# Kernel optimization log

Hardware: AMD Instinct MI355X
Metric: run time of the kernel (lower is better)

## Reference

```python
import jax, jax.numpy as jnp
import numpy as np

HID = 4
IN = 150
LAYERS = 4
OUT = 1
SEQ = 512
BATCH = 256


def setup_inputs() -> dict:
    key = jax.random.key(0)
    ks = jax.random.split(key, 12)
    s = 1.0 / np.sqrt(HID)  # PyTorch LSTM init scale
    inp = {
        "x": jax.random.normal(ks[0], (SEQ, BATCH, IN), dtype=jnp.float32),
        "w_ih0": jax.random.uniform(ks[1], (4 * HID, IN), minval=-s, maxval=s, dtype=jnp.float32),
        "w_hh0": jax.random.uniform(ks[2], (4 * HID, HID), minval=-s, maxval=s, dtype=jnp.float32),
        "b_ih0": jax.random.uniform(ks[3], (4 * HID,), minval=-s, maxval=s, dtype=jnp.float32),
        "b_hh0": jax.random.uniform(ks[4], (4 * HID,), minval=-s, maxval=s, dtype=jnp.float32),
        "w_ih_rest": jax.random.uniform(ks[5], (LAYERS - 1, 4 * HID, HID), minval=-s, maxval=s, dtype=jnp.float32),
        "w_hh_rest": jax.random.uniform(ks[6], (LAYERS - 1, 4 * HID, HID), minval=-s, maxval=s, dtype=jnp.float32),
        "b_ih_rest": jax.random.uniform(ks[7], (LAYERS - 1, 4 * HID), minval=-s, maxval=s, dtype=jnp.float32),
        "b_hh_rest": jax.random.uniform(ks[8], (LAYERS - 1, 4 * HID), minval=-s, maxval=s, dtype=jnp.float32),
        "fc_w": jax.random.uniform(ks[9], (OUT, HID), minval=-s, maxval=s, dtype=jnp.float32),
        "fc_b": jax.random.uniform(ks[10], (OUT,), minval=-s, maxval=s, dtype=jnp.float32),
    }
    return inp


def _lstm_layer(x, w_ih, w_hh, b_ih, b_hh):
    # x: (S, B, D_in). PyTorch gate order: i, f, g, o.
    B = x.shape[1]
    xp = jnp.einsum('sbd,gd->sbg', x, w_ih) + (b_ih + b_hh)  # (S, B, 4H)

    def step(carry, xt):
        h, c = carry
        gates = xt + h @ w_hh.T  # (B, 4H)
        i, f, g, o = jnp.split(gates, 4, axis=-1)
        i = jax.nn.sigmoid(i)
        f = jax.nn.sigmoid(f)
        g = jnp.tanh(g)
        o = jax.nn.sigmoid(o)
        c = f * c + i * g
        h = o * jnp.tanh(c)
        return (h, c), h

    h0 = jnp.zeros((B, HID), dtype=x.dtype)
    c0 = jnp.zeros((B, HID), dtype=x.dtype)
    _, hs = jax.lax.scan(step, (h0, c0), xp)
    return hs  # (S, B, H)


def reference(x, w_ih0, w_hh0, b_ih0, b_hh0, w_ih_rest, w_hh_rest, b_ih_rest, b_hh_rest, fc_w, fc_b):
    h = _lstm_layer(x, w_ih0, w_hh0, b_ih0, b_hh0)
    for l in range(LAYERS - 1):
        h = _lstm_layer(h, w_ih_rest[l], w_hh_rest[l], b_ih_rest[l], b_hh_rest[l])
    s, b, hd = h.shape
    out = h.reshape(s * b, hd) @ fc_w.T + fc_b  # (S*B, OUT)
    return out.reshape(s, b, -1)
```

## Files before the change

kernel.cpp:

```cpp
#include <hip/hip_runtime.h>
#include <hip/hip_bf16.h>

#define SEQ 512
#define BATCH 256
#define IN_DIM 150

#if __has_builtin(__builtin_amdgcn_exp2f)
__device__ __forceinline__ float fexp2(float x){ return __builtin_amdgcn_exp2f(x); }
#else
__device__ __forceinline__ float fexp2(float x){ return exp2f(x); }
#endif
#if __has_builtin(__builtin_amdgcn_rcpf)
__device__ __forceinline__ float frcp(float x){ return __builtin_amdgcn_rcpf(x); }
#else
__device__ __forceinline__ float frcp(float x){ return 1.0f/(x); }
#endif

__device__ __forceinline__ float sigm(float x){ return frcp(1.0f + fexp2(-1.44269504088896341f*x)); }
__device__ __forceinline__ float tanhx(float x){ return 1.0f - 2.0f*frcp(1.0f + fexp2(2.88539008177792681f*x)); }

template<int CTRL>
__device__ __forceinline__ float dppmov(float v){
    return __int_as_float(__builtin_amdgcn_mov_dpp(__float_as_int(v), CTRL, 0xF, 0xF, true));
}

__global__ __launch_bounds__(256) void xproj(const float* __restrict__ x,
                                             const float* __restrict__ w,
                                             const float* __restrict__ bih,
                                             const float* __restrict__ bhh,
                                             float* __restrict__ xp)
{
    __shared__ float wl[16*IN_DIM];
    __shared__ float bl[16];
    for (int i=threadIdx.x; i<16*IN_DIM; i+=256) wl[i] = w[i];
    if (threadIdx.x < 16) bl[threadIdx.x] = bih[threadIdx.x] + bhh[threadIdx.x];
    __syncthreads();

    const int r = blockIdx.x*256 + threadIdx.x;
    const float* xr = x + (size_t)r*IN_DIM;
    float acc[16];
#pragma unroll
    for (int g=0; g<16; ++g) acc[g] = bl[g];
#pragma unroll 5
    for (int dq=0; dq<IN_DIM/2; ++dq) {
        const float2 xv = *(const float2*)(xr + dq*2);
#pragma unroll
        for (int g=0; g<16; ++g) {
            const float2 wv = *(const float2*)(&wl[g*IN_DIM + dq*2]);
            acc[g] += xv.x*wv.x + xv.y*wv.y;
        }
    }
    float4* op = (float4*)(xp + (size_t)r*16);
#pragma unroll
    for (int kk=0; kk<4; ++kk)
        op[kk] = make_float4(acc[kk], acc[4+kk], acc[8+kk], acc[12+kk]);
}

__global__ __launch_bounds__(64) void lstm_pipe(
    const float* __restrict__ xp,
    const float* __restrict__ w_hh0,
    const float* __restrict__ w_ih_r,
    const float* __restrict__ w_hh_r,
    const float* __restrict__ b_ih_r,
    const float* __restrict__ b_hh_r,
    const float* __restrict__ fcw,
    const float* __restrict__ fcb,
    float* __restrict__ out)
{
    const int lane = threadIdx.x;
    const int k  = lane & 3;
    const int l  = (lane >> 2) & 3;
    const int bb = lane >> 4;
    const int b  = blockIdx.x*4 + bb;

    const float* whh = (l==0) ? w_hh0 : (w_hh_r + (size_t)(l-1)*64);
    float whp[4][4], wir[4][4], bias[4], fcp[4];
#pragma unroll
    for (int j=0;j<4;++j) {
        const int row = j*4+k;
#pragma unroll
        for (int m=0;m<4;++m) whp[j][m] = whh[row*4 + (k^m)];
        if (l==0) {
            bias[j] = 0.f;
#pragma unroll
            for (int m=0;m<4;++m) wir[j][m] = (m==j) ? 1.f : 0.f;
        } else {
            const float* wih = w_ih_r + (size_t)(l-1)*64;
            bias[j] = b_ih_r[(l-1)*16+row] + b_hh_r[(l-1)*16+row];
#pragma unroll
            for (int m=0;m<4;++m) wir[j][m] = wih[row*4 + (k^m)];
        }
    }
#pragma unroll
    for (int m=0;m<4;++m) fcp[m] = fcw[k^m];
    const float fcbv = fcb[0];

    const float* xbase = xp + (size_t)b*16 + k*4;

    float h=0.f, c=0.f;
    float a0=0.f,a1=0.f,a2=0.f,a3=0.f;
    float s0=0.f,s1=0.f,s2=0.f,s3=0.f;

    auto LDX = [&](int t)->float4 {
        const int tc = t < SEQ-1 ? t : SEQ-1;
        return *(const float4*)(xbase + (size_t)tc*(BATCH*16));
    };

    auto STEP = [&](float4 xv, int tau) {
        const float x0 = (l==0) ? xv.x : s0;
        const float x1 = (l==0) ? xv.y : s1;
        const float x2 = (l==0) ? xv.z : s2;
        const float x3 = (l==0) ? xv.w : s3;
        float g0 = (bias[0] + ((wir[0][0]*x0 + wir[0][1]*x1) + (wir[0][2]*x2 + wir[0][3]*x3)))
                 + ((whp[0][0]*a0 + whp[0][1]*a1) + (whp[0][2]*a2 + whp[0][3]*a3));
        float g1 = (bias[1] + ((wir[1][0]*x0 + wir[1][1]*x1) + (wir[1][2]*x2 + wir[1][3]*x3)))
                 + ((whp[1][0]*a0 + whp[1][1]*a1) + (whp[1][2]*a2 + whp[1][3]*a3));
        float g2 = (bias[2] + ((wir[2][0]*x0 + wir[2][1]*x1) + (wir[2][2]*x2 + wir[2][3]*x3)))
                 + ((whp[2][0]*a0 + whp[2][1]*a1) + (whp[2][2]*a2 + whp[2][3]*a3));
        float g3 = (bias[3] + ((wir[3][0]*x0 + wir[3][1]*x1) + (wir[3][2]*x2 + wir[3][3]*x3)))
                 + ((whp[3][0]*a0 + whp[3][1]*a1) + (whp[3][2]*a2 + whp[3][3]*a3));
        const float ig = sigm(g0);
        const float fg = sigm(g1);
        const float gg = tanhx(g2);
        const float og = sigm(g3);
        c = fg*c + ig*gg;
        h = og * tanhx(c);
        const int t = tau - l;
        if (t < 0) { h = 0.f; c = 0.f; }
        a0 = h;
        a1 = dppmov<0xB1>(h);
        a2 = dppmov<0x4E>(h);
        a3 = dppmov<0x1B>(h);
        s0 = dppmov<0x114>(a0);
        s1 = dppmov<0x114>(a1);
        s2 = dppmov<0x114>(a2);
        s3 = dppmov<0x114>(a3);
        if (l==3 && k==0 && t >= 0 && t < SEQ) {
            out[(size_t)t*BATCH + b] =
                fcbv + ((fcp[0]*a0 + fcp[1]*a1) + (fcp[2]*a2 + fcp[3]*a3));
        }
    };

    float4 A0=LDX(0), A1=LDX(1), A2=LDX(2), A3=LDX(3);
    for (int tau=0; tau<520; tau+=8) {
        float4 B0=LDX(tau+4), B1=LDX(tau+5), B2=LDX(tau+6), B3=LDX(tau+7);
        STEP(A0,tau);   STEP(A1,tau+1); STEP(A2,tau+2); STEP(A3,tau+3);
        A0=LDX(tau+8);  A1=LDX(tau+9);  A2=LDX(tau+10); A3=LDX(tau+11);
        STEP(B0,tau+4); STEP(B1,tau+5); STEP(B2,tau+6); STEP(B3,tau+7);
    }
}

extern "C" void kernel_launch(void* const* d_in, const int* in_sizes, int n_in,
                              void* d_out, int out_size, void* d_ws, size_t ws_size,
                              hipStream_t stream)
{
    const float* x      = (const float*)d_in[0];
    const float* w_ih0  = (const float*)d_in[1];
    const float* w_hh0  = (const float*)d_in[2];
    const float* b_ih0  = (const float*)d_in[3];
    const float* b_hh0  = (const float*)d_in[4];
    const float* w_ih_r = (const float*)d_in[5];
    const float* w_hh_r = (const float*)d_in[6];
    const float* b_ih_r = (const float*)d_in[7];
    const float* b_hh_r = (const float*)d_in[8];
    const float* fc_w   = (const float*)d_in[9];
    const float* fc_b   = (const float*)d_in[10];
    float* out = (float*)d_out;

    float* xp0 = (float*)d_ws;

    xproj<<<SEQ*BATCH/256, 256, 0, stream>>>(x, w_ih0, b_ih0, b_hh0, xp0);
    lstm_pipe<<<BATCH/4, 64, 0, stream>>>(xp0, w_hh0, w_ih_r, w_hh_r,
                                          b_ih_r, b_hh_r, fc_w, fc_b, out);
}
```

Measured before the change: 270.1 us.

## Interleave two batch groups per wave and prescale gate weights into exp2 domain

```diff
diff --git a/kernel.cpp b/kernel.cpp
--- a/kernel.cpp
+++ b/kernel.cpp
@@ -16,47 +16,106 @@
 __device__ __forceinline__ float frcp(float x){ return 1.0f/(x); }
 #endif
 
-__device__ __forceinline__ float sigm(float x){ return frcp(1.0f + fexp2(-1.44269504088896341f*x)); }
-__device__ __forceinline__ float tanhx(float x){ return 1.0f - 2.0f*frcp(1.0f + fexp2(2.88539008177792681f*x)); }
+#define NEG_LOG2E -1.44269504088896341f
+#define TWO_LOG2E  2.88539008177792681f
 
 template<int CTRL>
 __device__ __forceinline__ float dppmov(float v){
     return __int_as_float(__builtin_amdgcn_mov_dpp(__float_as_int(v), CTRL, 0xF, 0xF, true));
 }
 
-__global__ __launch_bounds__(256) void xproj(const float* __restrict__ x,
-                                             const float* __restrict__ w,
-                                             const float* __restrict__ bih,
-                                             const float* __restrict__ bhh,
-                                             float* __restrict__ xp)
-{
-    __shared__ float wl[16*IN_DIM];
-    __shared__ float bl[16];
-    for (int i=threadIdx.x; i<16*IN_DIM; i+=256) wl[i] = w[i];
-    if (threadIdx.x < 16) bl[threadIdx.x] = bih[threadIdx.x] + bhh[threadIdx.x];
+#define XROWS 64
+__global__ __launch_bounds__(256) void xproj2(const float* __restrict__ x,
+                                              const float* __restrict__ w,
+                                              const float* __restrict__ bih,
+                                              const float* __restrict__ bhh,
+                                              float* __restrict__ xp)
+{
+    __shared__ float xs[XROWS*IN_DIM];
+    __shared__ float ws[16*IN_DIM];
+    __shared__ float bs[16];
+
+    for (int i=threadIdx.x; i<16*IN_DIM; i+=256) ws[i] = w[i];
+    if (threadIdx.x < 16) bs[threadIdx.x] = bih[threadIdx.x] + bhh[threadIdx.x];
+
+    const size_t tilebase = (size_t)blockIdx.x * XROWS * IN_DIM;
+    const float2* xg  = (const float2*)(x + tilebase);
+    float2*       xs2 = (float2*)xs;
+    for (int i=threadIdx.x; i<XROWS*(IN_DIM/2); i+=256) xs2[i] = xg[i];
     __syncthreads();
 
-    const int r = blockIdx.x*256 + threadIdx.x;
-    const float* xr = x + (size_t)r*IN_DIM;
-    float acc[16];
-#pragma unroll
-    for (int g=0; g<16; ++g) acc[g] = bl[g];
+    const int q = threadIdx.x & 3;
+    const int r = threadIdx.x >> 2;
+    float acc0 = bs[q], acc1 = bs[4+q], acc2 = bs[8+q], acc3 = bs[12+q];
+    const float* xr = xs + r*IN_DIM;
+    const float* w0p = ws + (q    )*IN_DIM;
+    const float* w1p = ws + (q+ 4 )*IN_DIM;
+    const float* w2p = ws + (q+ 8 )*IN_DIM;
+    const float* w3p = ws + (q+12 )*IN_DIM;
 #pragma unroll 5
-    for (int dq=0; dq<IN_DIM/2; ++dq) {
-        const float2 xv = *(const float2*)(xr + dq*2);
-#pragma unroll
-        for (int g=0; g<16; ++g) {
-            const float2 wv = *(const float2*)(&wl[g*IN_DIM + dq*2]);
-            acc[g] += xv.x*wv.x + xv.y*wv.y;
-        }
-    }
-    float4* op = (float4*)(xp + (size_t)r*16);
-#pragma unroll
-    for (int kk=0; kk<4; ++kk)
-        op[kk] = make_float4(acc[kk], acc[4+kk], acc[8+kk], acc[12+kk]);
-}
-
-__global__ __launch_bounds__(64) void lstm_pipe(
+    for (int d=0; d<IN_DIM/2; ++d) {
+        const float2 xv = *(const float2*)(xr  + 2*d);
+        const float2 w0 = *(const float2*)(w0p + 2*d);
+        const float2 w1 = *(const float2*)(w1p + 2*d);
+        const float2 w2 = *(const float2*)(w2p + 2*d);
+        const float2 w3 = *(const float2*)(w3p + 2*d);
+        acc0 += xv.x*w0.x + xv.y*w0.y;
+        acc1 += xv.x*w1.x + xv.y*w1.y;
+        acc2 += xv.x*w2.x + xv.y*w2.y;
+        acc3 += xv.x*w3.x + xv.y*w3.y;
+    }
+    const float4 o = make_float4(acc0*NEG_LOG2E, acc1*NEG_LOG2E,
+                                 acc2*TWO_LOG2E, acc3*NEG_LOG2E);
+    *(float4*)(xp + ((size_t)(blockIdx.x*XROWS + r))*16 + q*4) = o;
+}
+
+template<int PHASE>
+__device__ __forceinline__ void lstm_step(
+    float& h, float& c,
+    float& a0, float& a1, float& a2, float& a3,
+    float& s0, float& s1, float& s2, float& s3,
+    const float4 xv, const int tau, const int l, const int k, const int b,
+    const float wir[4][4], const float whp[4][4], const float bias[4],
+    const float fcp[4], const float fcbv, float* __restrict__ out)
+{
+    const float x0 = (l==0) ? xv.x : s0;
+    const float x1 = (l==0) ? xv.y : s1;
+    const float x2 = (l==0) ? xv.z : s2;
+    const float x3 = (l==0) ? xv.w : s3;
+    float g0 = (bias[0] + ((wir[0][0]*x0 + wir[0][1]*x1) + (wir[0][2]*x2 + wir[0][3]*x3)))
+             + ((whp[0][0]*a0 + whp[0][1]*a1) + (whp[0][2]*a2 + whp[0][3]*a3));
+    float g1 = (bias[1] + ((wir[1][0]*x0 + wir[1][1]*x1) + (wir[1][2]*x2 + wir[1][3]*x3)))
+             + ((whp[1][0]*a0 + whp[1][1]*a1) + (whp[1][2]*a2 + whp[1][3]*a3));
+    float g2 = (bias[2] + ((wir[2][0]*x0 + wir[2][1]*x1) + (wir[2][2]*x2 + wir[2][3]*x3)))
+             + ((whp[2][0]*a0 + whp[2][1]*a1) + (whp[2][2]*a2 + whp[2][3]*a3));
+    float g3 = (bias[3] + ((wir[3][0]*x0 + wir[3][1]*x1) + (wir[3][2]*x2 + wir[3][3]*x3)))
+             + ((whp[3][0]*a0 + whp[3][1]*a1) + (whp[3][2]*a2 + whp[3][3]*a3));
+    const float ig = frcp(1.0f + fexp2(g0));
+    const float fg = frcp(1.0f + fexp2(g1));
+    const float rg = frcp(1.0f + fexp2(g2));
+    const float og = frcp(1.0f + fexp2(g3));
+    const float gg = __builtin_fmaf(-2.0f, rg, 1.0f);
+    c = __builtin_fmaf(fg, c, ig*gg);
+    const float rc = frcp(1.0f + fexp2(TWO_LOG2E*c));
+    h = og * __builtin_fmaf(-2.0f, rc, 1.0f);
+    const int t = tau - l;
+    if (PHASE==0) { if (t < 0) { h = 0.f; c = 0.f; } }
+    a0 = h;
+    a1 = dppmov<0xB1>(h);
+    a2 = dppmov<0x4E>(h);
+    a3 = dppmov<0x1B>(h);
+    s0 = dppmov<0x114>(a0);
+    s1 = dppmov<0x114>(a1);
+    s2 = dppmov<0x114>(a2);
+    s3 = dppmov<0x114>(a3);
+    bool doSt = (l==3) && (k==0);
+    if (PHASE==0) doSt = doSt && (t >= 0);
+    if (PHASE==2) doSt = doSt && (t < SEQ);
+    if (doSt) out[(size_t)t*BATCH + b] =
+        fcbv + ((fcp[0]*a0 + fcp[1]*a1) + (fcp[2]*a2 + fcp[3]*a3));
+}
+
+__global__ __launch_bounds__(64) void lstm_pipe2(
     const float* __restrict__ xp,
     const float* __restrict__ w_hh0,
     const float* __restrict__ w_ih_r,
@@ -71,83 +130,103 @@
     const int k  = lane & 3;
     const int l  = (lane >> 2) & 3;
     const int bb = lane >> 4;
-    const int b  = blockIdx.x*4 + bb;
 
     const float* whh = (l==0) ? w_hh0 : (w_hh_r + (size_t)(l-1)*64);
     float whp[4][4], wir[4][4], bias[4], fcp[4];
+    const float sfac[4] = {NEG_LOG2E, NEG_LOG2E, TWO_LOG2E, NEG_LOG2E};
 #pragma unroll
     for (int j=0;j<4;++j) {
         const int row = j*4+k;
-#pragma unroll
-        for (int m=0;m<4;++m) whp[j][m] = whh[row*4 + (k^m)];
+        const float sj = sfac[j];
+#pragma unroll
+        for (int m=0;m<4;++m) whp[j][m] = sj*whh[row*4 + (k^m)];
         if (l==0) {
             bias[j] = 0.f;
 #pragma unroll
             for (int m=0;m<4;++m) wir[j][m] = (m==j) ? 1.f : 0.f;
         } else {
             const float* wih = w_ih_r + (size_t)(l-1)*64;
-            bias[j] = b_ih_r[(l-1)*16+row] + b_hh_r[(l-1)*16+row];
-#pragma unroll
-            for (int m=0;m<4;++m) wir[j][m] = wih[row*4 + (k^m)];
+            bias[j] = sj*(b_ih_r[(l-1)*16+row] + b_hh_r[(l-1)*16+row]);
+#pragma unroll
+            for (int m=0;m<4;++m) wir[j][m] = sj*wih[row*4 + (k^m)];
         }
     }
 #pragma unroll
     for (int m=0;m<4;++m) fcp[m] = fcw[k^m];
     const float fcbv = fcb[0];
 
-    const float* xbase = xp + (size_t)b*16 + k*4;
-
-    float h=0.f, c=0.f;
-    float a0=0.f,a1=0.f,a2=0.f,a3=0.f;
-    float s0=0.f,s1=0.f,s2=0.f,s3=0.f;
-
-    auto LDX = [&](int t)->float4 {
-        const int tc = t < SEQ-1 ? t : SEQ-1;
-        return *(const float4*)(xbase + (size_t)tc*(BATCH*16));
-    };
-
-    auto STEP = [&](float4 xv, int tau) {
-        const float x0 = (l==0) ? xv.x : s0;
-        const float x1 = (l==0) ? xv.y : s1;
-        const float x2 = (l==0) ? xv.z : s2;
-        const float x3 = (l==0) ? xv.w : s3;
-        float g0 = (bias[0] + ((wir[0][0]*x0 + wir[0][1]*x1) + (wir[0][2]*x2 + wir[0][3]*x3)))
-                 + ((whp[0][0]*a0 + whp[0][1]*a1) + (whp[0][2]*a2 + whp[0][3]*a3));
-        float g1 = (bias[1] + ((wir[1][0]*x0 + wir[1][1]*x1) + (wir[1][2]*x2 + wir[1][3]*x3)))
-                 + ((whp[1][0]*a0 + whp[1][1]*a1) + (whp[1][2]*a2 + whp[1][3]*a3));
-        float g2 = (bias[2] + ((wir[2][0]*x0 + wir[2][1]*x1) + (wir[2][2]*x2 + wir[2][3]*x3)))
-                 + ((whp[2][0]*a0 + whp[2][1]*a1) + (whp[2][2]*a2 + whp[2][3]*a3));
-        float g3 = (bias[3] + ((wir[3][0]*x0 + wir[3][1]*x1) + (wir[3][2]*x2 + wir[3][3]*x3)))
-                 + ((whp[3][0]*a0 + whp[3][1]*a1) + (whp[3][2]*a2 + whp[3][3]*a3));
-        const float ig = sigm(g0);
-        const float fg = sigm(g1);
-        const float gg = tanhx(g2);
-        const float og = sigm(g3);
-        c = fg*c + ig*gg;
-        h = og * tanhx(c);
-        const int t = tau - l;
-        if (t < 0) { h = 0.f; c = 0.f; }
-        a0 = h;
-        a1 = dppmov<0xB1>(h);
-        a2 = dppmov<0x4E>(h);
-        a3 = dppmov<0x1B>(h);
-        s0 = dppmov<0x114>(a0);
-        s1 = dppmov<0x114>(a1);
-        s2 = dppmov<0x114>(a2);
-        s3 = dppmov<0x114>(a3);
-        if (l==3 && k==0 && t >= 0 && t < SEQ) {
-            out[(size_t)t*BATCH + b] =
-                fcbv + ((fcp[0]*a0 + fcp[1]*a1) + (fcp[2]*a2 + fcp[3]*a3));
-        }
-    };
-
-    float4 A0=LDX(0), A1=LDX(1), A2=LDX(2), A3=LDX(3);
-    for (int tau=0; tau<520; tau+=8) {
-        float4 B0=LDX(tau+4), B1=LDX(tau+5), B2=LDX(tau+6), B3=LDX(tau+7);
-        STEP(A0,tau);   STEP(A1,tau+1); STEP(A2,tau+2); STEP(A3,tau+3);
-        A0=LDX(tau+8);  A1=LDX(tau+9);  A2=LDX(tau+10); A3=LDX(tau+11);
-        STEP(B0,tau+4); STEP(B1,tau+5); STEP(B2,tau+6); STEP(B3,tau+7);
-    }
+    int bidx[2];
+    const float* xbase[2];
+#pragma unroll
+    for (int g=0; g<2; ++g) {
+        bidx[g]  = blockIdx.x*8 + g*4 + bb;
+        xbase[g] = xp + (size_t)bidx[g]*16 + k*4;
+    }
+    float H[2]={0.f,0.f}, C[2]={0.f,0.f};
+    float A0[2]={0,0},A1[2]={0,0},A2[2]={0,0},A3[2]={0,0};
+    float S0[2]={0,0},S1[2]={0,0},S2[2]={0,0},S3[2]={0,0};
+
+    float4 BA[2][4], BB[2][4];
+
+#define LDX(g,t)       (*(const float4*)(xbase[g] + (size_t)(t)*(BATCH*16)))
+#define LDXC(g,t)      (*(const float4*)(xbase[g] + (size_t)((t)<SEQ-1?(t):SEQ-1)*(BATCH*16)))
+#define STEP(P,g,buf,tau_) lstm_step<P>(H[g],C[g],A0[g],A1[g],A2[g],A3[g], \
+        S0[g],S1[g],S2[g],S3[g], buf, tau_, l, k, bidx[g], wir, whp, bias, fcp, fcbv, out)
+
+#pragma unroll
+    for (int g=0; g<2; ++g) {
+#pragma unroll
+        for (int j=0;j<4;++j) BA[g][j] = LDX(g, j);
+    }
+
+    {
+        const int tau = 0;
+#pragma unroll
+        for (int g=0; g<2; ++g) { BB[g][0]=LDX(g,tau+4); BB[g][1]=LDX(g,tau+5); BB[g][2]=LDX(g,tau+6); BB[g][3]=LDX(g,tau+7); }
+#pragma unroll
+        for (int j=0;j<4;++j)
+#pragma unroll
+            for (int g=0; g<2; ++g) STEP(0, g, BA[g][j], tau+j);
+#pragma unroll
+        for (int g=0; g<2; ++g) { BA[g][0]=LDX(g,tau+8); BA[g][1]=LDX(g,tau+9); BA[g][2]=LDX(g,tau+10); BA[g][3]=LDX(g,tau+11); }
+#pragma unroll
+        for (int j=0;j<4;++j)
+#pragma unroll
+            for (int g=0; g<2; ++g) STEP(0, g, BB[g][j], tau+4+j);
+    }
+
+    for (int tau=8; tau<496; tau+=8) {
+#pragma unroll
+        for (int g=0; g<2; ++g) { BB[g][0]=LDX(g,tau+4); BB[g][1]=LDX(g,tau+5); BB[g][2]=LDX(g,tau+6); BB[g][3]=LDX(g,tau+7); }
+#pragma unroll
+        for (int j=0;j<4;++j)
+#pragma unroll
+            for (int g=0; g<2; ++g) STEP(1, g, BA[g][j], tau+j);
+#pragma unroll
+        for (int g=0; g<2; ++g) { BA[g][0]=LDX(g,tau+8); BA[g][1]=LDX(g,tau+9); BA[g][2]=LDX(g,tau+10); BA[g][3]=LDX(g,tau+11); }
+#pragma unroll
+        for (int j=0;j<4;++j)
+#pragma unroll
+            for (int g=0; g<2; ++g) STEP(1, g, BB[g][j], tau+4+j);
+    }
+
+    for (int tau=496; tau<520; tau+=8) {
+#pragma unroll
+        for (int g=0; g<2; ++g) { BB[g][0]=LDXC(g,tau+4); BB[g][1]=LDXC(g,tau+5); BB[g][2]=LDXC(g,tau+6); BB[g][3]=LDXC(g,tau+7); }
+#pragma unroll
+        for (int j=0;j<4;++j)
+#pragma unroll
+            for (int g=0; g<2; ++g) STEP(2, g, BA[g][j], tau+j);
+#pragma unroll
+        for (int g=0; g<2; ++g) { BA[g][0]=LDXC(g,tau+8); BA[g][1]=LDXC(g,tau+9); BA[g][2]=LDXC(g,tau+10); BA[g][3]=LDXC(g,tau+11); }
+#pragma unroll
+        for (int j=0;j<4;++j)
+#pragma unroll
+            for (int g=0; g<2; ++g) STEP(2, g, BB[g][j], tau+4+j);
+    }
+#undef LDX
+#undef LDXC
+#undef STEP
 }
 
 extern "C" void kernel_launch(void* const* d_in, const int* in_sizes, int n_in,
@@ -169,7 +248,7 @@
 
     float* xp0 = (float*)d_ws;
 
-    xproj<<<SEQ*BATCH/256, 256, 0, stream>>>(x, w_ih0, b_ih0, b_hh0, xp0);
-    lstm_pipe<<<BATCH/4, 64, 0, stream>>>(xp0, w_hh0, w_ih_r, w_hh_r,
-                                          b_ih_r, b_hh_r, fc_w, fc_b, out);
-}
+    xproj2<<<SEQ*BATCH/XROWS, 256, 0, stream>>>(x, w_ih0, b_ih0, b_hh0, xp0);
+    lstm_pipe2<<<BATCH/8, 64, 0, stream>>>(xp0, w_hh0, w_ih_r, w_hh_r,
+                                           b_ih_r, b_hh_r, fc_w, fc_b, out);
+}
```

After: 384.4 us. +42.3%, slower.
